# Performance work log

Measured on AMD Instinct MI355X. Metric: run time of the kernel, lower is better.

The kernel has to match this reference:

```python
import jax, jax.numpy as jnp
import numpy as np

B, S, I, H, L1, O = 128, 1024, 256, 512, 256, 64

def _xavier(key, shape):
    fan_in, fan_out = shape[-2] if len(shape) > 1 else shape[-1], shape[-1]
    limit = float(np.sqrt(6.0 / (fan_in + fan_out)))
    return jax.random.uniform(key, shape, jnp.float32, -limit, limit)

def setup_inputs() -> dict:
    key = jax.random.key(0)
    ks = jax.random.split(key, 20)
    d = {"X": jax.random.normal(ks[0], (B, S, I), jnp.float32)}
    names = [("W_xi", (I, H)), ("W_hi", (H, H)), ("b_i", (1, H)),
             ("W_xf", (I, H)), ("W_hf", (H, H)), ("b_f", (1, H)),
             ("W_xo", (I, H)), ("W_ho", (H, H)), ("b_o", (1, H)),
             ("W_xc", (I, H)), ("W_hc", (H, H)), ("b_c", (1, H)),
             ("W_o1", (H, L1)), ("b_o1", (1, L1)), ("W_o2", (L1, O)), ("b_o2", (1, O))]
    for k, (n, shp) in zip(ks[1:], names):
        d[n] = _xavier(k, shp)
    return d

def reference(X, W_xi, W_hi, b_i, W_xf, W_hf, b_f, W_xo, W_ho, b_o, W_xc, W_hc, b_c, W_o1, b_o1, W_o2, b_o2):
    batch = X.shape[0]
    hid = W_hi.shape[0]
    # Precompute all input projections in one big GEMM: [B,S,4H]
    Wx = jnp.concatenate([W_xi, W_xf, W_xo, W_xc], axis=1)
    pre = jnp.einsum('bsi,ig->bsg', X, Wx)  # [B,S,4H]
    pre = jnp.transpose(pre, (1, 0, 2))     # [S,B,4H] for scan

    def step(carry, p):
        Hs, Cs = carry
        pi, pf, po, pc = jnp.split(p, 4, axis=-1)
        Ig = jax.nn.sigmoid(pi + Hs @ W_hi + b_i)
        Fg = jax.nn.sigmoid(pf + Hs @ W_hf + b_f)
        Og = jax.nn.sigmoid(po + Hs @ W_ho + b_o)
        Ct = jnp.tanh(pc + Hs @ W_hc + b_c)
        Cn = Fg * Cs + Ig * Ct
        # NOTE: original module uses tanh(C) + O (addition), not O * tanh(C)
        Hn = jnp.tanh(Cn) + Og
        return (Hn, Cn), None

    H0 = jnp.zeros((batch, hid), X.dtype)
    C0 = jnp.zeros((batch, hid), X.dtype)
    (Hf, Cf), _ = jax.lax.scan(step, (H0, C0), pre)
    # Output head: only the final timestep's output is returned by the loop
    h1 = jax.nn.relu(Hf @ W_o1 + b_o1)
    output = jax.nn.softmax(h1 @ W_o2 + b_o2, axis=1)
    return output, Hf, Cf
```

## Files before the change

kernel.cpp:

```cpp
#include <hip/hip_runtime.h>

#define B_   128
#define S_   1024
#define I_   256
#define H_   512
#define L1_  256
#define O_   64

#define NGRP 8
#define WGPG 32
#define MB   16
#define NH   16
#define SX   8
#define SH   16

#define HB_UINTS_PER_BUF 32768

typedef __attribute__((ext_vector_type(8))) short short8;
typedef __attribute__((ext_vector_type(4))) float f4;
typedef __attribute__((ext_vector_type(4))) unsigned u32x4;

__device__ __forceinline__ unsigned short f2bf(float x) {
  unsigned u = __builtin_bit_cast(unsigned, x);
  u += 0x7FFFu + ((u >> 16) & 1u);
  return (unsigned short)(u >> 16);
}

__device__ __forceinline__ f4 mfma_bf16(short8 a, short8 b, f4 c) {
  asm("v_mfma_f32_16x16x32_bf16 %0, %1, %2, %0" : "+v"(c) : "v"(a), "v"(b));
  return c;
}

__device__ __forceinline__ void stage_chunk(unsigned short* dst, f4 a, f4 b) {
  unsigned d0, d1, d2, d3;
  asm("v_cvt_pk_bf16_f32 %0, %1, %2" : "=v"(d0) : "v"(a[0]), "v"(a[1]));
  asm("v_cvt_pk_bf16_f32 %0, %1, %2" : "=v"(d1) : "v"(a[2]), "v"(a[3]));
  asm("v_cvt_pk_bf16_f32 %0, %1, %2" : "=v"(d2) : "v"(b[0]), "v"(b[1]));
  asm("v_cvt_pk_bf16_f32 %0, %1, %2" : "=v"(d3) : "v"(b[2]), "v"(b[3]));
  u32x4 v = {d0, d1, d2, d3};
  *(u32x4*)dst = v;
}

__global__ __launch_bounds__(256, 1)
void lstm_rec(const float* __restrict__ X,
              const float* __restrict__ Wxi, const float* __restrict__ Whi, const float* __restrict__ bi,
              const float* __restrict__ Wxf, const float* __restrict__ Whf, const float* __restrict__ bfp,
              const float* __restrict__ Wxo, const float* __restrict__ Who, const float* __restrict__ bop,
              const float* __restrict__ Wxc, const float* __restrict__ Whc, const float* __restrict__ bcp,
              float* __restrict__ out, unsigned* __restrict__ flags,
              unsigned* __restrict__ xslots, unsigned* __restrict__ Hbuf)
{
  __shared__ unsigned short WhF[4][SH][64][8];
  __shared__ unsigned short WxF[4][SX][64][8];
  __shared__ unsigned short AsH[SH][64][8];
  __shared__ float Psw[4][16][20];
  __shared__ int mode_s;

  const int tid  = threadIdx.x;
  const int lane = tid & 63;
  const int wv   = tid >> 6;
  const int g    = blockIdx.x & 7;
  const int jg   = blockIdx.x >> 3;
  const int j0   = jg * NH;
  const int b0   = g * MB;

  unsigned xcc;
  asm volatile("s_getreg_b32 %0, hwreg(HW_REG_XCC_ID)" : "=s"(xcc));
  xcc &= 15u;
  if (tid == 0)
    __hip_atomic_store(xslots + g * 32 + jg, xcc + 1u,
                       __ATOMIC_RELAXED, __HIP_MEMORY_SCOPE_AGENT);

  const int idxA = tid, idxB = 256 + tid;
  const int sA = idxA >> 6, posA = idxA & 63;
  const int sB = idxB >> 6, posB = idxB & 63;
  const int offA = (sA * 64 + posA) * 8;
  const int offB = (sB * 64 + posB) * 8;
  const float* bpa = X + (size_t)(b0 + (posA & 15)) * S_ * I_ + (sA * 32 + (posA >> 4) * 8);
  const float* bpb = X + (size_t)(b0 + (posB & 15)) * S_ * I_ + (sB * 32 + (posB >> 4) * 8);
  f4 ra0 = *(const f4*)(bpa);
  f4 ra1 = *(const f4*)(bpa + 4);
  f4 rb0 = *(const f4*)(bpb);
  f4 rb1 = *(const f4*)(bpb + 4);

  const float* Whg[4] = {Whi, Whf, Who, Whc};
  const float* Wxg[4] = {Wxi, Wxf, Wxo, Wxc};
  const float* bgp[4] = {bi, bfp, bop, bcp};

  for (int gate = 0; gate < 4; ++gate) {
    const float* Wp = Whg[gate];
    for (int it = 0; it < 32; ++it) {
      int idx = it * 256 + tid;
      int k = idx >> 4, c = idx & 15;
      WhF[gate][k >> 5][((k & 31) >> 3) * 16 + c][k & 7] = f2bf(Wp[(size_t)k * H_ + j0 + c]);
    }
    const float* Xp = Wxg[gate];
    for (int it = 0; it < 16; ++it) {
      int idx = it * 256 + tid;
      int k = idx >> 4, c = idx & 15;
      WxF[gate][k >> 5][((k & 31) >> 3) * 16 + c][k & 7] = f2bf(Xp[(size_t)k * H_ + j0 + c]);
    }
  }
  if (tid == 0) mode_s = 0;
  __syncthreads();

  const int colL  = lane & 15;
  const int rgrpL = lane >> 4;
  const int gateL = colL >> 2;
  const int ccL   = colL & 3;
  short8 wx[SX], wh[SH];
  #pragma unroll
  for (int s = 0; s < SX; ++s)
    wx[s] = *(const short8*)&WxF[gateL][s][rgrpL * 16 + wv * 4 + ccL][0];
  #pragma unroll
  for (int s = 0; s < SH; ++s)
    wh[s] = *(const short8*)&WhF[gateL][s][rgrpL * 16 + wv * 4 + ccL][0];
  const float bv = bgp[gateL][j0 + wv * 4 + ccL];

  if (wv == 0) {
    unsigned v;
    for (;;) {
      v = __hip_atomic_load(xslots + g * 32 + (lane & 31),
                            __ATOMIC_RELAXED, __HIP_MEMORY_SCOPE_AGENT);
      if (__all((int)(v != 0u))) break;
      __builtin_amdgcn_s_sleep(1);
    }
    unsigned f0 = (unsigned)__shfl((int)v, 0, 64);
    int same = __all((int)(v == f0));
    if (lane == 0) mode_s = same;
  }
  __syncthreads();
  const bool l2m = (mode_s != 0);

  unsigned short* axbase = &WxF[0][0][0][0];
  const int AXSTRIDE = SX * 64 * 8;
  stage_chunk(axbase + offA, ra0, ra1);
  stage_chunk(axbase + offB, rb0, rb1);
  __syncthreads();

  float Creg = 0.f;
  const int rowG = lane >> 2;
  const int cG   = lane & 3;
  const int jG   = j0 + wv * 4 + cG;
  const int dwH  = (((jG >> 5) * 64) + ((jG >> 3) & 3) * 16 + rowG) * 4 + ((jG & 7) >> 1);

  unsigned* myflags = flags + g * 32;
  const unsigned* fp0 = myflags + (lane & 31);

  for (int t = 0; t < S_; ++t) {
    const bool last = (t == S_ - 1);

    unsigned fpre = 0u;
    if (t > 0)
      asm volatile("global_load_dword %0, %1, off sc0 sc1"
                   : "+v"(fpre) : "v"(fp0) : "memory");

    f4 acc0 = {bv, bv, bv, bv};
    f4 acc1 = {0.f, 0.f, 0.f, 0.f};
    asm("s_nop 1" : "+v"(acc0));
    asm("s_nop 1" : "+v"(acc1));
    const unsigned short* ax = axbase + (t & 1) * AXSTRIDE;
    #pragma unroll
    for (int s = 0; s < SX; ++s) {
      short8 a = *(const short8*)(ax + (s * 64 + lane) * 8);
      if (s & 1) acc1 = mfma_bf16(a, wx[s], acc1);
      else       acc0 = mfma_bf16(a, wx[s], acc0);
    }

    if (t > 0) {
      asm volatile("s_waitcnt vmcnt(0)" : "+v"(fpre) :: "memory");
      __builtin_amdgcn_sched_barrier(0);
      if (!__all((int)(fpre >= (unsigned)t))) {
        for (;;) {
          unsigned v = __hip_atomic_load(fp0, __ATOMIC_RELAXED, __HIP_MEMORY_SCOPE_AGENT);
          if (__all((int)(v >= (unsigned)t))) break;
          __builtin_amdgcn_s_sleep(1);
        }
      }
      const u32x4* gp = (const u32x4*)(Hbuf + (size_t)(t & 1) * HB_UINTS_PER_BUF + g * 4096);
      u32x4 r0, r1, r2, r3;
      if (l2m) {
        asm volatile(
          "global_load_dwordx4 %0, %4, off sc0\n\t"
          "global_load_dwordx4 %1, %5, off sc0\n\t"
          "global_load_dwordx4 %2, %6, off sc0\n\t"
          "global_load_dwordx4 %3, %7, off sc0\n\t"
          "s_waitcnt vmcnt(0)"
          : "=&v"(r0), "=&v"(r1), "=&v"(r2), "=&v"(r3)
          : "v"(gp + tid), "v"(gp + tid + 256), "v"(gp + tid + 512), "v"(gp + tid + 768)
          : "memory");
      } else {
        asm volatile(
          "global_load_dwordx4 %0, %4, off sc0 sc1\n\t"
          "global_load_dwordx4 %1, %5, off sc0 sc1\n\t"
          "global_load_dwordx4 %2, %6, off sc0 sc1\n\t"
          "global_load_dwordx4 %3, %7, off sc0 sc1\n\t"
          "s_waitcnt vmcnt(0)"
          : "=&v"(r0), "=&v"(r1), "=&v"(r2), "=&v"(r3)
          : "v"(gp + tid), "v"(gp + tid + 256), "v"(gp + tid + 512), "v"(gp + tid + 768)
          : "memory");
      }
      u32x4* lp = (u32x4*)&AsH[0][0][0];
      lp[tid]       = r0;
      lp[tid + 256] = r1;
      lp[tid + 512] = r2;
      lp[tid + 768] = r3;
    }
    __syncthreads();

    if (!last) {
      const float* pa  = bpa + (size_t)(t + 1) * I_;
      const float* pb2 = bpb + (size_t)(t + 1) * I_;
      ra0 = *(const f4*)(pa);
      ra1 = *(const f4*)(pa + 4);
      rb0 = *(const f4*)(pb2);
      rb1 = *(const f4*)(pb2 + 4);
    }

    if (t > 0) {
      #pragma unroll
      for (int s = 0; s < SH; ++s) {
        short8 a = *(const short8*)&AsH[s][lane][0];
        if (s & 1) acc1 = mfma_bf16(a, wh[s], acc1);
        else       acc0 = mfma_bf16(a, wh[s], acc0);
      }
    }
    asm("s_nop 7" : "+v"(acc0));
    asm("s_nop 7" : "+v"(acc1));
    f4 accs = {acc0[0] + acc1[0], acc0[1] + acc1[1], acc0[2] + acc1[2], acc0[3] + acc1[3]};

    *(f4*)&Psw[wv][colL][rgrpL * 4] = accs;
    asm volatile("s_waitcnt lgkmcnt(0)" ::: "memory");
    __builtin_amdgcn_sched_barrier(0);
    float pi = Psw[wv][cG][rowG];
    float pf = Psw[wv][4 + cG][rowG];
    float po = Psw[wv][8 + cG][rowG];
    float pc = Psw[wv][12 + cG][rowG];

    float Ig = 1.f / (1.f + __expf(-pi));
    float Fg = 1.f / (1.f + __expf(-pf));
    float Og = 1.f / (1.f + __expf(-po));
    float Ct = 1.f - 2.f / (__expf(2.f * pc) + 1.f);
    float Cn = Fg * Creg + Ig * Ct;
    Creg = Cn;
    float Hn = (1.f - 2.f / (__expf(2.f * Cn) + 1.f)) + Og;

    if (!last) {
      unsigned short* axw = axbase + ((t + 1) & 1) * AXSTRIDE;
      stage_chunk(axw + offA, ra0, ra1);
      stage_chunk(axw + offB, rb0, rb1);

      float Hp = __shfl_xor(Hn, 1, 64);
      if ((cG & 1) == 0) {
        unsigned packed;
        asm("v_cvt_pk_bf16_f32 %0, %1, %2" : "=v"(packed) : "v"(Hn), "v"(Hp));
        unsigned* dst = Hbuf + (size_t)((t + 1) & 1) * HB_UINTS_PER_BUF + g * 4096 + dwH;
        if (l2m)
          asm volatile("global_store_dword %0, %1, off sc0" :: "v"(dst), "v"(packed) : "memory");
        else
          asm volatile("global_store_dword %0, %1, off sc0 sc1" :: "v"(dst), "v"(packed) : "memory");
      }
      __syncthreads();
      if (tid == 0)
        __hip_atomic_store(myflags + jg, (unsigned)(t + 1),
                           __ATOMIC_RELAXED, __HIP_MEMORY_SCOPE_AGENT);
    } else {
      out[B_ * O_ + (size_t)(b0 + rowG) * H_ + jG] = Hn;
      out[B_ * O_ + B_ * H_ + (size_t)(b0 + rowG) * H_ + jG] = Cn;
    }
  }
}

__global__ __launch_bounds__(256, 1)
void lstm_head(const float* __restrict__ Hf,
               const float* __restrict__ Wo1, const float* __restrict__ bo1,
               const float* __restrict__ Wo2, const float* __restrict__ bo2,
               float* __restrict__ outp)
{
  __shared__ float hf[H_];
  __shared__ float h1[L1_];
  const int tid = threadIdx.x;
  const int b = blockIdx.x;
  hf[tid]       = Hf[(size_t)b * H_ + tid];
  hf[tid + 256] = Hf[(size_t)b * H_ + tid + 256];
  __syncthreads();
  float a = bo1[tid];
  #pragma unroll 8
  for (int k = 0; k < H_; ++k) a = fmaf(hf[k], Wo1[(size_t)k * L1_ + tid], a);
  h1[tid] = fmaxf(a, 0.f);
  __syncthreads();
  if (tid < O_) {
    float l = bo2[tid];
    #pragma unroll 8
    for (int j = 0; j < L1_; ++j) l = fmaf(h1[j], Wo2[(size_t)j * O_ + tid], l);
    float m = l;
    #pragma unroll
    for (int off = 32; off > 0; off >>= 1) m = fmaxf(m, __shfl_xor(m, off, 64));
    float e = __expf(l - m);
    float ssum = e;
    #pragma unroll
    for (int off = 32; off > 0; off >>= 1) ssum += __shfl_xor(ssum, off, 64);
    outp[(size_t)b * O_ + tid] = e / ssum;
  }
}

extern "C" void kernel_launch(void* const* d_in, const int* in_sizes, int n_in,
                              void* d_out, int out_size, void* d_ws, size_t ws_size,
                              hipStream_t stream) {
  (void)in_sizes; (void)n_in; (void)out_size; (void)ws_size;
  const float* X   = (const float*)d_in[0];
  const float* Wxi = (const float*)d_in[1];
  const float* Whi = (const float*)d_in[2];
  const float* bi  = (const float*)d_in[3];
  const float* Wxf = (const float*)d_in[4];
  const float* Whf = (const float*)d_in[5];
  const float* bfv = (const float*)d_in[6];
  const float* Wxo = (const float*)d_in[7];
  const float* Who = (const float*)d_in[8];
  const float* bo  = (const float*)d_in[9];
  const float* Wxc = (const float*)d_in[10];
  const float* Whc = (const float*)d_in[11];
  const float* bc  = (const float*)d_in[12];
  const float* Wo1 = (const float*)d_in[13];
  const float* bo1 = (const float*)d_in[14];
  const float* Wo2 = (const float*)d_in[15];
  const float* bo2 = (const float*)d_in[16];
  float* out = (float*)d_out;

  unsigned* flags  = (unsigned*)d_ws;
  unsigned* xslots = (unsigned*)((char*)d_ws + 1024);
  unsigned* Hbuf   = (unsigned*)((char*)d_ws + 2048);

  (void)hipMemsetAsync(d_ws, 0, 2048, stream);
  hipLaunchKernelGGL(lstm_rec, dim3(NGRP * WGPG), dim3(256), 0, stream,
                     X, Wxi, Whi, bi, Wxf, Whf, bfv, Wxo, Who, bo, Wxc, Whc, bc,
                     out, flags, xslots, Hbuf);
  hipLaunchKernelGGL(lstm_head, dim3(B_), dim3(256), 0, stream,
                     out + B_ * O_, Wo1, bo1, Wo2, bo2, out);
}
```

Baseline: 2.164 ms.

## Use per-group atomic counter barrier in L2 mode and split MFMA accumulators

In L2-local mode, the per-step inter-workgroup barrier becomes a single atomic counter per batch group: each workgroup atomically increments it, and one lane polls it with atomic-or reads. That lane then releases the other waves through an LDS flag instead of every lane polling 32 flag words. The MFMA accumulation is also split across four accumulators rather than two, to shorten the dependent MFMA chains. The risks are contention on a single atomic address and the extra intra-block spin on LDS.

```diff
diff --git a/kernel.cpp b/kernel.cpp
--- a/kernel.cpp
+++ b/kernel.cpp
@@ -48,13 +48,15 @@
               const float* __restrict__ Wxo, const float* __restrict__ Who, const float* __restrict__ bop,
               const float* __restrict__ Wxc, const float* __restrict__ Whc, const float* __restrict__ bcp,
               float* __restrict__ out, unsigned* __restrict__ flags,
-              unsigned* __restrict__ xslots, unsigned* __restrict__ Hbuf)
+              unsigned* __restrict__ xslots, unsigned* __restrict__ cnts,
+              unsigned* __restrict__ Hbuf)
 {
   __shared__ unsigned short WhF[4][SH][64][8];
   __shared__ unsigned short WxF[4][SX][64][8];
   __shared__ unsigned short AsH[SH][64][8];
   __shared__ float Psw[4][16][20];
   __shared__ int mode_s;
+  __shared__ int go_s;
 
   const int tid  = threadIdx.x;
   const int lane = tid & 63;
@@ -101,7 +103,7 @@
       WxF[gate][k >> 5][((k & 31) >> 3) * 16 + c][k & 7] = f2bf(Xp[(size_t)k * H_ + j0 + c]);
     }
   }
-  if (tid == 0) mode_s = 0;
+  if (tid == 0) { mode_s = 0; go_s = 0; }
   __syncthreads();
 
   const int colL  = lane & 15;
@@ -146,35 +148,74 @@
 
   unsigned* myflags = flags + g * 32;
   const unsigned* fp0 = myflags + (lane & 31);
+  unsigned* myflagp = myflags + jg;
+  unsigned* gcnt = cnts + g * 32;
 
   for (int t = 0; t < S_; ++t) {
     const bool last = (t == S_ - 1);
 
     unsigned fpre = 0u;
-    if (t > 0)
-      asm volatile("global_load_dword %0, %1, off sc0 sc1"
-                   : "+v"(fpre) : "v"(fp0) : "memory");
+    unsigned cpre = 0u;
+    if (t > 0) {
+      if (l2m) {
+        if (wv == 0 && lane == 0)
+          asm volatile("global_atomic_or %0, %1, %2, off sc0"
+                       : "+v"(cpre) : "v"(gcnt), "v"(0u) : "memory");
+      } else {
+        asm volatile("global_load_dword %0, %1, off sc0 sc1"
+                     : "+v"(fpre) : "v"(fp0) : "memory");
+      }
+    }
 
     f4 acc0 = {bv, bv, bv, bv};
     f4 acc1 = {0.f, 0.f, 0.f, 0.f};
-    asm("s_nop 1" : "+v"(acc0));
-    asm("s_nop 1" : "+v"(acc1));
+    f4 acc2 = {0.f, 0.f, 0.f, 0.f};
+    f4 acc3 = {0.f, 0.f, 0.f, 0.f};
+    asm("s_nop 1" : "+v"(acc0), "+v"(acc1), "+v"(acc2), "+v"(acc3));
     const unsigned short* ax = axbase + (t & 1) * AXSTRIDE;
     #pragma unroll
     for (int s = 0; s < SX; ++s) {
       short8 a = *(const short8*)(ax + (s * 64 + lane) * 8);
-      if (s & 1) acc1 = mfma_bf16(a, wx[s], acc1);
-      else       acc0 = mfma_bf16(a, wx[s], acc0);
+      switch (s & 3) {
+        case 0: acc0 = mfma_bf16(a, wx[s], acc0); break;
+        case 1: acc1 = mfma_bf16(a, wx[s], acc1); break;
+        case 2: acc2 = mfma_bf16(a, wx[s], acc2); break;
+        default: acc3 = mfma_bf16(a, wx[s], acc3); break;
+      }
     }
 
     if (t > 0) {
-      asm volatile("s_waitcnt vmcnt(0)" : "+v"(fpre) :: "memory");
-      __builtin_amdgcn_sched_barrier(0);
-      if (!__all((int)(fpre >= (unsigned)t))) {
-        for (;;) {
-          unsigned v = __hip_atomic_load(fp0, __ATOMIC_RELAXED, __HIP_MEMORY_SCOPE_AGENT);
-          if (__all((int)(v >= (unsigned)t))) break;
-          __builtin_amdgcn_s_sleep(1);
+      if (l2m) {
+        const unsigned target = 32u * (unsigned)t;
+        if (wv == 0) {
+          asm volatile("s_waitcnt vmcnt(0)" : "+v"(cpre) :: "memory");
+          __builtin_amdgcn_sched_barrier(0);
+          if (lane == 0) {
+            if (cpre < target) {
+              for (;;) {
+                unsigned v;
+                asm volatile("global_atomic_or %0, %1, %2, off sc0\n\t"
+                             "s_waitcnt vmcnt(0)"
+                             : "=v"(v) : "v"(gcnt), "v"(0u) : "memory");
+                if (v >= target) break;
+                __builtin_amdgcn_s_sleep(1);
+              }
+            }
+            __builtin_amdgcn_sched_barrier(0);
+            *(volatile int*)&go_s = t;
+          }
+        } else {
+          while (*(volatile int*)&go_s < t) __builtin_amdgcn_s_sleep(1);
+        }
+      } else {
+        asm volatile("s_waitcnt vmcnt(0)" : "+v"(fpre) :: "memory");
+        __builtin_amdgcn_sched_barrier(0);
+        if (!__all((int)(fpre >= (unsigned)t))) {
+          for (;;) {
+            unsigned v = __hip_atomic_load(fp0, __ATOMIC_RELAXED, __HIP_MEMORY_SCOPE_AGENT);
+            if (__all((int)(v >= (unsigned)t))) break;
+            __builtin_amdgcn_s_sleep(1);
+          }
         }
       }
       const u32x4* gp = (const u32x4*)(Hbuf + (size_t)(t & 1) * HB_UINTS_PER_BUF + g * 4096);
@@ -221,13 +262,18 @@
       #pragma unroll
       for (int s = 0; s < SH; ++s) {
         short8 a = *(const short8*)&AsH[s][lane][0];
-        if (s & 1) acc1 = mfma_bf16(a, wh[s], acc1);
-        else       acc0 = mfma_bf16(a, wh[s], acc0);
-      }
-    }
-    asm("s_nop 7" : "+v"(acc0));
-    asm("s_nop 7" : "+v"(acc1));
-    f4 accs = {acc0[0] + acc1[0], acc0[1] + acc1[1], acc0[2] + acc1[2], acc0[3] + acc1[3]};
+        switch (s & 3) {
+          case 0: acc0 = mfma_bf16(a, wh[s], acc0); break;
+          case 1: acc1 = mfma_bf16(a, wh[s], acc1); break;
+          case 2: acc2 = mfma_bf16(a, wh[s], acc2); break;
+          default: acc3 = mfma_bf16(a, wh[s], acc3); break;
+        }
+      }
+    }
+    asm("s_nop 7\n\ts_nop 7" : "+v"(acc0), "+v"(acc1), "+v"(acc2), "+v"(acc3));
+    f4 s01 = {acc0[0] + acc1[0], acc0[1] + acc1[1], acc0[2] + acc1[2], acc0[3] + acc1[3]};
+    f4 s23 = {acc2[0] + acc3[0], acc2[1] + acc3[1], acc2[2] + acc3[2], acc2[3] + acc3[3]};
+    f4 accs = {s01[0] + s23[0], s01[1] + s23[1], s01[2] + s23[2], s01[3] + s23[3]};
 
     *(f4*)&Psw[wv][colL][rgrpL * 4] = accs;
     asm volatile("s_waitcnt lgkmcnt(0)" ::: "memory");
@@ -261,9 +307,16 @@
           asm volatile("global_store_dword %0, %1, off sc0 sc1" :: "v"(dst), "v"(packed) : "memory");
       }
       __syncthreads();
-      if (tid == 0)
-        __hip_atomic_store(myflags + jg, (unsigned)(t + 1),
-                           __ATOMIC_RELAXED, __HIP_MEMORY_SCOPE_AGENT);
+      if (tid == 0) {
+        if (l2m) {
+          asm volatile("global_atomic_add %0, %1, off"
+                       :: "v"(gcnt), "v"(1u) : "memory");
+        } else {
+          unsigned tv = (unsigned)(t + 1);
+          asm volatile("global_store_dword %0, %1, off sc0 sc1"
+                       :: "v"(myflagp), "v"(tv) : "memory");
+        }
+      }
     } else {
       out[B_ * O_ + (size_t)(b0 + rowG) * H_ + jG] = Hn;
       out[B_ * O_ + B_ * H_ + (size_t)(b0 + rowG) * H_ + jG] = Cn;
@@ -329,12 +382,13 @@
 
   unsigned* flags  = (unsigned*)d_ws;
   unsigned* xslots = (unsigned*)((char*)d_ws + 1024);
-  unsigned* Hbuf   = (unsigned*)((char*)d_ws + 2048);
-
-  (void)hipMemsetAsync(d_ws, 0, 2048, stream);
+  unsigned* cnts   = (unsigned*)((char*)d_ws + 2048);
+  unsigned* Hbuf   = (unsigned*)((char*)d_ws + 4096);
+
+  (void)hipMemsetAsync(d_ws, 0, 4096, stream);
   hipLaunchKernelGGL(lstm_rec, dim3(NGRP * WGPG), dim3(256), 0, stream,
                      X, Wxi, Whi, bi, Wxf, Whf, bfv, Wxo, Who, bo, Wxc, Whc, bc,
-                     out, flags, xslots, Hbuf);
+                     out, flags, xslots, cnts, Hbuf);
   hipLaunchKernelGGL(lstm_head, dim3(B_), dim3(256), 0, stream,
                      out + B_ * O_, Wo1, bo1, Wo2, bo2, out);
 }
```

Result: slower. 2.348 ms (+8.5%).

## Use per-wave completion flags and four MFMA accumulator chains in LSTM step

Applied to the files above, without the earlier changes.

Each wave now publishes its own step flag right after its H stores drain, instead of one flag per workgroup set after a block barrier. Consumers poll 128 per-group flags with two loads per lane. The flag store and H store now complete before the x-chunk staging and the __syncthreads, which removes the barrier from the critical producer path. MFMA accumulation is also split across four independent accumulator chains instead of two to shorten dependency stalls, at the cost of more polling traffic and extra registers.

```diff
diff --git a/kernel.cpp b/kernel.cpp
--- a/kernel.cpp
+++ b/kernel.cpp
@@ -144,36 +144,48 @@
   const int jG   = j0 + wv * 4 + cG;
   const int dwH  = (((jG >> 5) * 64) + ((jG >> 3) & 3) * 16 + rowG) * 4 + ((jG & 7) >> 1);
 
-  unsigned* myflags = flags + g * 32;
-  const unsigned* fp0 = myflags + (lane & 31);
+  unsigned* gflags = flags + g * 128;
+  const unsigned* fpA = gflags + lane;
+  const unsigned* fpB = gflags + 64 + lane;
+  unsigned* myflagp = gflags + jg * 4 + wv;
 
   for (int t = 0; t < S_; ++t) {
     const bool last = (t == S_ - 1);
 
-    unsigned fpre = 0u;
+    unsigned fa = 0u, fb = 0u;
     if (t > 0)
-      asm volatile("global_load_dword %0, %1, off sc0 sc1"
-                   : "+v"(fpre) : "v"(fp0) : "memory");
+      asm volatile("global_load_dword %0, %2, off sc0 sc1\n\t"
+                   "global_load_dword %1, %3, off sc0 sc1"
+                   : "+v"(fa), "+v"(fb) : "v"(fpA), "v"(fpB) : "memory");
 
     f4 acc0 = {bv, bv, bv, bv};
     f4 acc1 = {0.f, 0.f, 0.f, 0.f};
-    asm("s_nop 1" : "+v"(acc0));
-    asm("s_nop 1" : "+v"(acc1));
+    f4 acc2 = {0.f, 0.f, 0.f, 0.f};
+    f4 acc3 = {0.f, 0.f, 0.f, 0.f};
+    asm("s_nop 1" : "+v"(acc0), "+v"(acc1), "+v"(acc2), "+v"(acc3));
     const unsigned short* ax = axbase + (t & 1) * AXSTRIDE;
     #pragma unroll
     for (int s = 0; s < SX; ++s) {
       short8 a = *(const short8*)(ax + (s * 64 + lane) * 8);
-      if (s & 1) acc1 = mfma_bf16(a, wx[s], acc1);
-      else       acc0 = mfma_bf16(a, wx[s], acc0);
+      switch (s & 3) {
+        case 0: acc0 = mfma_bf16(a, wx[s], acc0); break;
+        case 1: acc1 = mfma_bf16(a, wx[s], acc1); break;
+        case 2: acc2 = mfma_bf16(a, wx[s], acc2); break;
+        default: acc3 = mfma_bf16(a, wx[s], acc3); break;
+      }
     }
 
     if (t > 0) {
-      asm volatile("s_waitcnt vmcnt(0)" : "+v"(fpre) :: "memory");
+      asm volatile("s_waitcnt vmcnt(0)" : "+v"(fa), "+v"(fb) :: "memory");
       __builtin_amdgcn_sched_barrier(0);
-      if (!__all((int)(fpre >= (unsigned)t))) {
+      if (!__all((int)((fa >= (unsigned)t) & (fb >= (unsigned)t)))) {
         for (;;) {
-          unsigned v = __hip_atomic_load(fp0, __ATOMIC_RELAXED, __HIP_MEMORY_SCOPE_AGENT);
-          if (__all((int)(v >= (unsigned)t))) break;
+          unsigned v1, v2;
+          asm volatile("global_load_dword %0, %2, off sc0 sc1\n\t"
+                       "global_load_dword %1, %3, off sc0 sc1\n\t"
+                       "s_waitcnt vmcnt(0)"
+                       : "=v"(v1), "=v"(v2) : "v"(fpA), "v"(fpB) : "memory");
+          if (__all((int)((v1 >= (unsigned)t) & (v2 >= (unsigned)t)))) break;
           __builtin_amdgcn_s_sleep(1);
         }
       }
@@ -221,13 +233,18 @@
       #pragma unroll
       for (int s = 0; s < SH; ++s) {
         short8 a = *(const short8*)&AsH[s][lane][0];
-        if (s & 1) acc1 = mfma_bf16(a, wh[s], acc1);
-        else       acc0 = mfma_bf16(a, wh[s], acc0);
-      }
-    }
-    asm("s_nop 7" : "+v"(acc0));
-    asm("s_nop 7" : "+v"(acc1));
-    f4 accs = {acc0[0] + acc1[0], acc0[1] + acc1[1], acc0[2] + acc1[2], acc0[3] + acc1[3]};
+        switch (s & 3) {
+          case 0: acc0 = mfma_bf16(a, wh[s], acc0); break;
+          case 1: acc1 = mfma_bf16(a, wh[s], acc1); break;
+          case 2: acc2 = mfma_bf16(a, wh[s], acc2); break;
+          default: acc3 = mfma_bf16(a, wh[s], acc3); break;
+        }
+      }
+    }
+    asm("s_nop 7\n\ts_nop 7" : "+v"(acc0), "+v"(acc1), "+v"(acc2), "+v"(acc3));
+    f4 s01 = {acc0[0] + acc1[0], acc0[1] + acc1[1], acc0[2] + acc1[2], acc0[3] + acc1[3]};
+    f4 s23 = {acc2[0] + acc3[0], acc2[1] + acc3[1], acc2[2] + acc3[2], acc2[3] + acc3[3]};
+    f4 accs = {s01[0] + s23[0], s01[1] + s23[1], s01[2] + s23[2], s01[3] + s23[3]};
 
     *(f4*)&Psw[wv][colL][rgrpL * 4] = accs;
     asm volatile("s_waitcnt lgkmcnt(0)" ::: "memory");
@@ -246,10 +263,6 @@
     float Hn = (1.f - 2.f / (__expf(2.f * Cn) + 1.f)) + Og;
 
     if (!last) {
-      unsigned short* axw = axbase + ((t + 1) & 1) * AXSTRIDE;
-      stage_chunk(axw + offA, ra0, ra1);
-      stage_chunk(axw + offB, rb0, rb1);
-
       float Hp = __shfl_xor(Hn, 1, 64);
       if ((cG & 1) == 0) {
         unsigned packed;
@@ -260,10 +273,17 @@
         else
           asm volatile("global_store_dword %0, %1, off sc0 sc1" :: "v"(dst), "v"(packed) : "memory");
       }
+      asm volatile("s_waitcnt vmcnt(0)" ::: "memory");
+      if (lane == 0) {
+        unsigned tv = (unsigned)(t + 1);
+        asm volatile("global_store_dword %0, %1, off sc0 sc1"
+                     :: "v"(myflagp), "v"(tv) : "memory");
+      }
+      unsigned short* axw = axbase + ((t + 1) & 1) * AXSTRIDE;
+      stage_chunk(axw + offA, ra0, ra1);
+      stage_chunk(axw + offB, rb0, rb1);
+
       __syncthreads();
-      if (tid == 0)
-        __hip_atomic_store(myflags + jg, (unsigned)(t + 1),
-                           __ATOMIC_RELAXED, __HIP_MEMORY_SCOPE_AGENT);
     } else {
       out[B_ * O_ + (size_t)(b0 + rowG) * H_ + jG] = Hn;
       out[B_ * O_ + B_ * H_ + (size_t)(b0 + rowG) * H_ + jG] = Cn;
@@ -328,10 +348,10 @@
   float* out = (float*)d_out;
 
   unsigned* flags  = (unsigned*)d_ws;
-  unsigned* xslots = (unsigned*)((char*)d_ws + 1024);
-  unsigned* Hbuf   = (unsigned*)((char*)d_ws + 2048);
-
-  (void)hipMemsetAsync(d_ws, 0, 2048, stream);
+  unsigned* xslots = (unsigned*)((char*)d_ws + 4096);
+  unsigned* Hbuf   = (unsigned*)((char*)d_ws + 8192);
+
+  (void)hipMemsetAsync(d_ws, 0, 8192, stream);
   hipLaunchKernelGGL(lstm_rec, dim3(NGRP * WGPG), dim3(256), 0, stream,
                      X, Wxi, Whi, bi, Wxf, Whf, bfv, Wxo, Who, bo, Wxc, Whc, bc,
                      out, flags, xslots, Hbuf);
```

After: 2.484 ms. +14.8%, slower.

## Split batch into 16 groups of 8 rows with 512 persistent workgroups

Applied to the files above, without the earlier changes.

Doubles the number of batch groups (each now 8 rows, zero-padded to the 16-row MFMA tile) so 512 workgroups run at two per CU. Weights are converted straight from global memory into registers, which drops the large LDS weight staging and leaves room for the second resident workgroup. Each workgroup now moves half as much H and X data per step, but half of every MFMA tile is padding. The cross-XCC path now always uses sc0 sc1 loads, and every step still synchronises 32 workgroups per group through flags.

```diff
diff --git a/kernel.cpp b/kernel.cpp
--- a/kernel.cpp
+++ b/kernel.cpp
@@ -7,14 +7,15 @@
 #define L1_  256
 #define O_   64
 
-#define NGRP 8
+#define NGRP 16
 #define WGPG 32
-#define MB   16
+#define MB   8
 #define NH   16
 #define SX   8
 #define SH   16
 
-#define HB_UINTS_PER_BUF 32768
+#define HB_UINTS_PER_GRP 2048
+#define HB_UINTS_PER_BUF (NGRP * HB_UINTS_PER_GRP)
 
 typedef __attribute__((ext_vector_type(8))) short short8;
 typedef __attribute__((ext_vector_type(4))) float f4;
@@ -41,7 +42,7 @@
   *(u32x4*)dst = v;
 }
 
-__global__ __launch_bounds__(256, 1)
+__global__ __launch_bounds__(256, 2)
 void lstm_rec(const float* __restrict__ X,
               const float* __restrict__ Wxi, const float* __restrict__ Whi, const float* __restrict__ bi,
               const float* __restrict__ Wxf, const float* __restrict__ Whf, const float* __restrict__ bfp,
@@ -50,8 +51,7 @@
               float* __restrict__ out, unsigned* __restrict__ flags,
               unsigned* __restrict__ xslots, unsigned* __restrict__ Hbuf)
 {
-  __shared__ unsigned short WhF[4][SH][64][8];
-  __shared__ unsigned short WxF[4][SX][64][8];
+  __shared__ unsigned short AsX[2][SX][64][8];
   __shared__ unsigned short AsH[SH][64][8];
   __shared__ float Psw[4][16][20];
   __shared__ int mode_s;
@@ -59,8 +59,8 @@
   const int tid  = threadIdx.x;
   const int lane = tid & 63;
   const int wv   = tid >> 6;
-  const int g    = blockIdx.x & 7;
-  const int jg   = blockIdx.x >> 3;
+  const int g    = blockIdx.x & 15;
+  const int jg   = blockIdx.x >> 4;
   const int j0   = jg * NH;
   const int b0   = g * MB;
 
@@ -71,51 +71,45 @@
     __hip_atomic_store(xslots + g * 32 + jg, xcc + 1u,
                        __ATOMIC_RELAXED, __HIP_MEMORY_SCOPE_AGENT);
 
-  const int idxA = tid, idxB = 256 + tid;
-  const int sA = idxA >> 6, posA = idxA & 63;
-  const int sB = idxB >> 6, posB = idxB & 63;
-  const int offA = (sA * 64 + posA) * 8;
-  const int offB = (sB * 64 + posB) * 8;
-  const float* bpa = X + (size_t)(b0 + (posA & 15)) * S_ * I_ + (sA * 32 + (posA >> 4) * 8);
-  const float* bpb = X + (size_t)(b0 + (posB & 15)) * S_ * I_ + (sB * 32 + (posB >> 4) * 8);
+  const int sA   = tid >> 5;
+  const int pkA  = (tid >> 3) & 3;
+  const int rowA = tid & 7;
+  const int offA = (sA * 64 + pkA * 16 + rowA) * 8;
+  const float* bpa = X + (size_t)(b0 + rowA) * S_ * I_ + sA * 32 + pkA * 8;
   f4 ra0 = *(const f4*)(bpa);
   f4 ra1 = *(const f4*)(bpa + 4);
-  f4 rb0 = *(const f4*)(bpb);
-  f4 rb1 = *(const f4*)(bpb + 4);
 
   const float* Whg[4] = {Whi, Whf, Who, Whc};
   const float* Wxg[4] = {Wxi, Wxf, Wxo, Wxc};
   const float* bgp[4] = {bi, bfp, bop, bcp};
-
-  for (int gate = 0; gate < 4; ++gate) {
-    const float* Wp = Whg[gate];
-    for (int it = 0; it < 32; ++it) {
-      int idx = it * 256 + tid;
-      int k = idx >> 4, c = idx & 15;
-      WhF[gate][k >> 5][((k & 31) >> 3) * 16 + c][k & 7] = f2bf(Wp[(size_t)k * H_ + j0 + c]);
-    }
-    const float* Xp = Wxg[gate];
-    for (int it = 0; it < 16; ++it) {
-      int idx = it * 256 + tid;
-      int k = idx >> 4, c = idx & 15;
-      WxF[gate][k >> 5][((k & 31) >> 3) * 16 + c][k & 7] = f2bf(Xp[(size_t)k * H_ + j0 + c]);
-    }
-  }
-  if (tid == 0) mode_s = 0;
-  __syncthreads();
 
   const int colL  = lane & 15;
   const int rgrpL = lane >> 4;
   const int gateL = colL >> 2;
   const int ccL   = colL & 3;
+  if (tid == 0) mode_s = 0;
+
+  const float* WhP = Whg[gateL];
+  const float* WxP = Wxg[gateL];
+  const int jcol = j0 + wv * 4 + ccL;
   short8 wx[SX], wh[SH];
   #pragma unroll
-  for (int s = 0; s < SX; ++s)
-    wx[s] = *(const short8*)&WxF[gateL][s][rgrpL * 16 + wv * 4 + ccL][0];
+  for (int s = 0; s < SH; ++s) {
+    union { unsigned short us[8]; short8 v; } t8;
+    #pragma unroll
+    for (int e = 0; e < 8; ++e)
+      t8.us[e] = f2bf(WhP[(size_t)(s * 32 + rgrpL * 8 + e) * H_ + jcol]);
+    wh[s] = t8.v;
+  }
   #pragma unroll
-  for (int s = 0; s < SH; ++s)
-    wh[s] = *(const short8*)&WhF[gateL][s][rgrpL * 16 + wv * 4 + ccL][0];
-  const float bv = bgp[gateL][j0 + wv * 4 + ccL];
+  for (int s = 0; s < SX; ++s) {
+    union { unsigned short us[8]; short8 v; } t8;
+    #pragma unroll
+    for (int e = 0; e < 8; ++e)
+      t8.us[e] = f2bf(WxP[(size_t)(s * 32 + rgrpL * 8 + e) * H_ + jcol]);
+    wx[s] = t8.v;
+  }
+  const float bv = bgp[gateL][jcol];
 
   if (wv == 0) {
     unsigned v;
@@ -132,20 +126,33 @@
   __syncthreads();
   const bool l2m = (mode_s != 0);
 
-  unsigned short* axbase = &WxF[0][0][0][0];
+  unsigned short* axbase = &AsX[0][0][0][0];
   const int AXSTRIDE = SX * 64 * 8;
+  const u32x4 zz = {0u, 0u, 0u, 0u};
+  #pragma unroll
+  for (int it = 0; it < 2; ++it) {
+    int idx = it * 256 + tid;
+    *(u32x4*)&AsH[idx >> 5][((idx >> 3) & 3) * 16 + 8 + (idx & 7)][0] = zz;
+  }
+  #pragma unroll
+  for (int it = 0; it < 2; ++it) {
+    int idx = it * 256 + tid;
+    int buf = idx >> 8, rem = idx & 255;
+    *(u32x4*)(axbase + buf * AXSTRIDE
+              + ((rem >> 5) * 64 + ((rem >> 3) & 3) * 16 + 8 + (rem & 7)) * 8) = zz;
+  }
   stage_chunk(axbase + offA, ra0, ra1);
-  stage_chunk(axbase + offB, rb0, rb1);
   __syncthreads();
 
   float Creg = 0.f;
   const int rowG = lane >> 2;
   const int cG   = lane & 3;
   const int jG   = j0 + wv * 4 + cG;
-  const int dwH  = (((jG >> 5) * 64) + ((jG >> 3) & 3) * 16 + rowG) * 4 + ((jG & 7) >> 1);
+  const int dwH  = ((jG >> 5) * 32 + ((jG >> 3) & 3) * 8 + rowG) * 4 + ((jG & 7) >> 1);
 
   unsigned* myflags = flags + g * 32;
   const unsigned* fp0 = myflags + (lane & 31);
+  unsigned* myflagp = myflags + jg;
 
   for (int t = 0; t < S_; ++t) {
     const bool last = (t == S_ - 1);
@@ -177,44 +184,26 @@
           __builtin_amdgcn_s_sleep(1);
         }
       }
-      const u32x4* gp = (const u32x4*)(Hbuf + (size_t)(t & 1) * HB_UINTS_PER_BUF + g * 4096);
-      u32x4 r0, r1, r2, r3;
-      if (l2m) {
-        asm volatile(
-          "global_load_dwordx4 %0, %4, off sc0\n\t"
-          "global_load_dwordx4 %1, %5, off sc0\n\t"
-          "global_load_dwordx4 %2, %6, off sc0\n\t"
-          "global_load_dwordx4 %3, %7, off sc0\n\t"
-          "s_waitcnt vmcnt(0)"
-          : "=&v"(r0), "=&v"(r1), "=&v"(r2), "=&v"(r3)
-          : "v"(gp + tid), "v"(gp + tid + 256), "v"(gp + tid + 512), "v"(gp + tid + 768)
-          : "memory");
-      } else {
-        asm volatile(
-          "global_load_dwordx4 %0, %4, off sc0 sc1\n\t"
-          "global_load_dwordx4 %1, %5, off sc0 sc1\n\t"
-          "global_load_dwordx4 %2, %6, off sc0 sc1\n\t"
-          "global_load_dwordx4 %3, %7, off sc0 sc1\n\t"
-          "s_waitcnt vmcnt(0)"
-          : "=&v"(r0), "=&v"(r1), "=&v"(r2), "=&v"(r3)
-          : "v"(gp + tid), "v"(gp + tid + 256), "v"(gp + tid + 512), "v"(gp + tid + 768)
-          : "memory");
-      }
-      u32x4* lp = (u32x4*)&AsH[0][0][0];
-      lp[tid]       = r0;
-      lp[tid + 256] = r1;
-      lp[tid + 512] = r2;
-      lp[tid + 768] = r3;
+      const u32x4* gp = (const u32x4*)(Hbuf + (size_t)(t & 1) * HB_UINTS_PER_BUF
+                                       + g * HB_UINTS_PER_GRP);
+      u32x4 r0, r1;
+      asm volatile(
+        "global_load_dwordx4 %0, %2, off sc0 sc1\n\t"
+        "global_load_dwordx4 %1, %3, off sc0 sc1\n\t"
+        "s_waitcnt vmcnt(0)"
+        : "=&v"(r0), "=&v"(r1)
+        : "v"(gp + tid), "v"(gp + tid + 256)
+        : "memory");
+      int c0 = tid, c1 = tid + 256;
+      *(u32x4*)&AsH[c0 >> 5][((c0 >> 3) & 3) * 16 + (c0 & 7)][0] = r0;
+      *(u32x4*)&AsH[c1 >> 5][((c1 >> 3) & 3) * 16 + (c1 & 7)][0] = r1;
     }
     __syncthreads();
 
     if (!last) {
-      const float* pa  = bpa + (size_t)(t + 1) * I_;
-      const float* pb2 = bpb + (size_t)(t + 1) * I_;
+      const float* pa = bpa + (size_t)(t + 1) * I_;
       ra0 = *(const f4*)(pa);
       ra1 = *(const f4*)(pa + 4);
-      rb0 = *(const f4*)(pb2);
-      rb1 = *(const f4*)(pb2 + 4);
     }
 
     if (t > 0) {
@@ -246,15 +235,14 @@
     float Hn = (1.f - 2.f / (__expf(2.f * Cn) + 1.f)) + Og;
 
     if (!last) {
-      unsigned short* axw = axbase + ((t + 1) & 1) * AXSTRIDE;
-      stage_chunk(axw + offA, ra0, ra1);
-      stage_chunk(axw + offB, rb0, rb1);
+      stage_chunk(axbase + ((t + 1) & 1) * AXSTRIDE + offA, ra0, ra1);
 
       float Hp = __shfl_xor(Hn, 1, 64);
-      if ((cG & 1) == 0) {
+      if ((cG & 1) == 0 && rowG < MB) {
         unsigned packed;
         asm("v_cvt_pk_bf16_f32 %0, %1, %2" : "=v"(packed) : "v"(Hn), "v"(Hp));
-        unsigned* dst = Hbuf + (size_t)((t + 1) & 1) * HB_UINTS_PER_BUF + g * 4096 + dwH;
+        unsigned* dst = Hbuf + (size_t)((t + 1) & 1) * HB_UINTS_PER_BUF
+                      + g * HB_UINTS_PER_GRP + dwH;
         if (l2m)
           asm volatile("global_store_dword %0, %1, off sc0" :: "v"(dst), "v"(packed) : "memory");
         else
@@ -262,9 +250,9 @@
       }
       __syncthreads();
       if (tid == 0)
-        __hip_atomic_store(myflags + jg, (unsigned)(t + 1),
+        __hip_atomic_store(myflagp, (unsigned)(t + 1),
                            __ATOMIC_RELAXED, __HIP_MEMORY_SCOPE_AGENT);
-    } else {
+    } else if (rowG < MB) {
       out[B_ * O_ + (size_t)(b0 + rowG) * H_ + jG] = Hn;
       out[B_ * O_ + B_ * H_ + (size_t)(b0 + rowG) * H_ + jG] = Cn;
     }
@@ -328,10 +316,10 @@
   float* out = (float*)d_out;
 
   unsigned* flags  = (unsigned*)d_ws;
-  unsigned* xslots = (unsigned*)((char*)d_ws + 1024);
-  unsigned* Hbuf   = (unsigned*)((char*)d_ws + 2048);
-
-  (void)hipMemsetAsync(d_ws, 0, 2048, stream);
+  unsigned* xslots = (unsigned*)((char*)d_ws + 2048);
+  unsigned* Hbuf   = (unsigned*)((char*)d_ws + 4096);
+
+  (void)hipMemsetAsync(d_ws, 0, 4096, stream);
   hipLaunchKernelGGL(lstm_rec, dim3(NGRP * WGPG), dim3(256), 0, stream,
                      X, Wxi, Whi, bi, Wxf, Whf, bfv, Wxo, Who, bo, Wxc, Whc, bc,
                      out, flags, xslots, Hbuf);
```

New measurement: 2.869 ms. 1.33x slower.
